# Optimization experiments

Measured on AMD Instinct MI355X. Metric: run time of the kernel, lower is better.

The kernel has to match this reference:

```python
import jax, jax.numpy as jnp
import numpy as np

N_ATOMS = 200_000
N_BONDS = 400_000
DEG = 2            # each bond receives from exactly 2 atoms (a2b edges)
D = 128


def setup_inputs() -> dict:
    key = jax.random.key(0)
    k1, k2, k3 = jax.random.split(key, 3)
    atom_ft = jax.random.normal(k1, (N_ATOMS, D), dtype=jnp.float32)
    bond_ft = jax.random.normal(k2, (N_BONDS, D), dtype=jnp.float32)
    edge_src = jax.random.randint(k3, (N_BONDS * DEG,), 0, N_ATOMS, dtype=jnp.int32)
    # every bond has exactly DEG incoming a2b edges -> dst is sorted repeats
    edge_dst = jnp.repeat(jnp.arange(N_BONDS, dtype=jnp.int32), DEG)
    return {"atom_ft": atom_ft, "bond_ft": bond_ft,
            "edge_src": edge_src, "edge_dst": edge_dst}


def reference(atom_ft, bond_ft, edge_src, edge_dst):
    """copy_u gather -> per-dst-segment mean and max -> concat with dst feats."""
    n_bonds = bond_ft.shape[0]
    msgs = atom_ft[edge_src]                                        # [E, D] gather
    seg_sum = jax.ops.segment_sum(msgs, edge_dst, num_segments=n_bonds)   # [n_bonds, D]
    cnt = jax.ops.segment_sum(jnp.ones((msgs.shape[0],), msgs.dtype),
                              edge_dst, num_segments=n_bonds)             # [n_bonds]
    mean_v = seg_sum / jnp.maximum(cnt, 1.0)[:, None]
    max_v = jax.ops.segment_max(msgs, edge_dst, num_segments=n_bonds)
    max_v = jnp.where(cnt[:, None] > 0, max_v, 0.0)  # guard empty segments
    return jnp.concatenate((bond_ft, mean_v, max_v), axis=1)        # [n_bonds, 3D]
```

## Files before the change

### kernel.cpp

```cpp
#include <hip/hip_runtime.h>


#define D 128
#define OUT_D (3 * D)

__global__ __launch_bounds__(256) void concat_mean_max_kernel(
    const float* __restrict__ atom_ft,
    const float* __restrict__ bond_ft,
    const int*  __restrict__ edge_src,
    float* __restrict__ out,
    int n_bonds)
{
    const int gid  = blockIdx.x * blockDim.x + threadIdx.x;
    const int bond = gid >> 5;
    const int lane = gid & 31;
    if (bond >= n_bonds) return;

    const int s0 = edge_src[2 * bond];
    const int s1 = edge_src[2 * bond + 1];

    const float4* a0 = (const float4*)(atom_ft + (size_t)s0 * D);
    const float4* a1 = (const float4*)(atom_ft + (size_t)s1 * D);
    const float4* bf = (const float4*)(bond_ft + (size_t)bond * D);

    const float4 v0 = a0[lane];
    const float4 v1 = a1[lane];
    const float4 b  = bf[lane];

    float4 mean, mx;
    mean.x = (v0.x + v1.x) * 0.5f;
    mean.y = (v0.y + v1.y) * 0.5f;
    mean.z = (v0.z + v1.z) * 0.5f;
    mean.w = (v0.w + v1.w) * 0.5f;
    mx.x = fmaxf(v0.x, v1.x);
    mx.y = fmaxf(v0.y, v1.y);
    mx.z = fmaxf(v0.z, v1.z);
    mx.w = fmaxf(v0.w, v1.w);

    float4* orow = (float4*)(out + (size_t)bond * OUT_D);
    orow[lane]      = b;
    orow[32 + lane] = mean;
    orow[64 + lane] = mx;
}

extern "C" void kernel_launch(void* const* d_in, const int* in_sizes, int n_in,
                              void* d_out, int out_size, void* d_ws, size_t ws_size,
                              hipStream_t stream) {
    const float* atom_ft  = (const float*)d_in[0];
    const float* bond_ft  = (const float*)d_in[1];
    const int*   edge_src = (const int*)d_in[2];
    float* out = (float*)d_out;

    const int n_bonds = in_sizes[1] / D;

    const int threads = 256;
    const int total   = n_bonds * 32;
    const int blocks  = (total + threads - 1) / threads;

    concat_mean_max_kernel<<<blocks, threads, 0, stream>>>(
        atom_ft, bond_ft, edge_src, out, n_bonds);
}
```

Measured before the change: 803.9 us.

## Process four bonds per group in a persistent grid-stride loop with index prefetch

Each 32-lane group now handles four bonds per iteration in a grid-stride loop over a capped grid of 2048 blocks. It prefetches the next iteration's edge_src indices while the current gathers are in flight. Bond features are read and all outputs written with nontemporal hints so streaming traffic does not pollute cache. The aim is more memory-level parallelism per thread and hidden index-load latency, at the cost of more registers and clamped duplicate writes on the tail.

Measured after the change: 794.2 us. Within noise of the previous version (-1.2%).

```diff
diff --git a/kernel.cpp b/kernel.cpp
--- a/kernel.cpp
+++ b/kernel.cpp
@@ -1,46 +1,79 @@
 #include <hip/hip_runtime.h>
 
 
-#define D 128
-#define OUT_D (3 * D)
+#define D      128
+#define OUT_D  (3 * D)
+#define BPG    4
+#define THREADS 256
 
-__global__ __launch_bounds__(256) void concat_mean_max_kernel(
+typedef float vfloat4 __attribute__((ext_vector_type(4)));
+
+__global__ __launch_bounds__(THREADS, 4) void concat_mean_max_kernel(
     const float* __restrict__ atom_ft,
     const float* __restrict__ bond_ft,
     const int*  __restrict__ edge_src,
     float* __restrict__ out,
     int n_bonds)
 {
-    const int gid  = blockIdx.x * blockDim.x + threadIdx.x;
-    const int bond = gid >> 5;
-    const int lane = gid & 31;
-    if (bond >= n_bonds) return;
+    const int lane   = threadIdx.x & 31;
+    const int grp    = blockIdx.x * (THREADS >> 5) + (threadIdx.x >> 5);
+    const int ngrp   = gridDim.x * (THREADS >> 5);
+    const int stride = ngrp * BPG;
 
-    const int s0 = edge_src[2 * bond];
-    const int s1 = edge_src[2 * bond + 1];
+    int base = grp * BPG;
+    if (base >= n_bonds) return;
 
-    const float4* a0 = (const float4*)(atom_ft + (size_t)s0 * D);
-    const float4* a1 = (const float4*)(atom_ft + (size_t)s1 * D);
-    const float4* bf = (const float4*)(bond_ft + (size_t)bond * D);
+    int s[2 * BPG];
+#pragma unroll
+    for (int j = 0; j < BPG; ++j) {
+        int b  = base + j;
+        int bb = (b < n_bonds) ? b : (n_bonds - 1);
+        s[2 * j]     = edge_src[2 * bb];
+        s[2 * j + 1] = edge_src[2 * bb + 1];
+    }
 
-    const float4 v0 = a0[lane];
-    const float4 v1 = a1[lane];
-    const float4 b  = bf[lane];
+    while (true) {
+        vfloat4 v0[BPG], v1[BPG], bf[BPG];
+        int bb[BPG];
+#pragma unroll
+        for (int j = 0; j < BPG; ++j) {
+            int b = base + j;
+            bb[j] = (b < n_bonds) ? b : (n_bonds - 1);
+            v0[j] = ((const vfloat4*)(atom_ft + (size_t)s[2 * j]     * D))[lane];
+            v1[j] = ((const vfloat4*)(atom_ft + (size_t)s[2 * j + 1] * D))[lane];
+            bf[j] = __builtin_nontemporal_load(
+                        ((const vfloat4*)(bond_ft + (size_t)bb[j] * D)) + lane);
+        }
 
-    float4 mean, mx;
-    mean.x = (v0.x + v1.x) * 0.5f;
-    mean.y = (v0.y + v1.y) * 0.5f;
-    mean.z = (v0.z + v1.z) * 0.5f;
-    mean.w = (v0.w + v1.w) * 0.5f;
-    mx.x = fmaxf(v0.x, v1.x);
-    mx.y = fmaxf(v0.y, v1.y);
-    mx.z = fmaxf(v0.z, v1.z);
-    mx.w = fmaxf(v0.w, v1.w);
+        const int next = base + stride;
+        if (next < n_bonds) {
+#pragma unroll
+            for (int j = 0; j < BPG; ++j) {
+                int b  = next + j;
+                int nb = (b < n_bonds) ? b : (n_bonds - 1);
+                s[2 * j]     = edge_src[2 * nb];
+                s[2 * j + 1] = edge_src[2 * nb + 1];
+            }
+        }
 
-    float4* orow = (float4*)(out + (size_t)bond * OUT_D);
-    orow[lane]      = b;
-    orow[32 + lane] = mean;
-    orow[64 + lane] = mx;
+#pragma unroll
+        for (int j = 0; j < BPG; ++j) {
+            vfloat4 mean = (v0[j] + v1[j]) * 0.5f;
+            vfloat4 mx;
+            mx.x = fmaxf(v0[j].x, v1[j].x);
+            mx.y = fmaxf(v0[j].y, v1[j].y);
+            mx.z = fmaxf(v0[j].z, v1[j].z);
+            mx.w = fmaxf(v0[j].w, v1[j].w);
+
+            vfloat4* orow = (vfloat4*)(out + (size_t)bb[j] * OUT_D);
+            __builtin_nontemporal_store(bf[j], orow + lane);
+            __builtin_nontemporal_store(mean,  orow + 32 + lane);
+            __builtin_nontemporal_store(mx,    orow + 64 + lane);
+        }
+
+        base = next;
+        if (base >= n_bonds) break;
+    }
 }
 
 extern "C" void kernel_launch(void* const* d_in, const int* in_sizes, int n_in,
@@ -53,10 +86,10 @@
 
     const int n_bonds = in_sizes[1] / D;
 
-    const int threads = 256;
-    const int total   = n_bonds * 32;
-    const int blocks  = (total + threads - 1) / threads;
+    const int groups_needed = (n_bonds + BPG - 1) / BPG;
+    const int blocks_full   = (groups_needed + (THREADS >> 5) - 1) / (THREADS >> 5);
+    const int blocks        = blocks_full < 2048 ? blocks_full : 2048;
 
-    concat_mean_max_kernel<<<blocks, threads, 0, stream>>>(
+    concat_mean_max_kernel<<<blocks, THREADS, 0, stream>>>(
         atom_ft, bond_ft, edge_src, out, n_bonds);
 }
```
